# Performance work log

Hardware: AMD Instinct MI355X
Metric: run time of the kernel (lower is better)

The kernel has to match this reference:

```python
import jax, jax.numpy as jnp
import numpy as np

N_BITS = 8
LEVELS = 2 ** N_BITS - 1  # 255 quantization levels (asymmetric uniform)
EPS = 1e-8


def _round_ste(x):
    # straight-through round (forward: round, backward: identity)
    return x + jax.lax.stop_gradient(jnp.round(x) - x)


def _fake_quant_uniform(x):
    # dynamic per-tensor asymmetric uniform quantization (UniformQuantizer)
    xmin = jnp.min(x)
    xmax = jnp.max(x)
    scale = jnp.maximum((xmax - xmin) / LEVELS, EPS)
    zero_point = jnp.round(-xmin / scale)
    x_int = jnp.clip(_round_ste(x / scale) + zero_point, 0, LEVELS)
    return (x_int - zero_point) * scale


def setup_inputs() -> dict:
    key = jax.random.key(0)
    kA, kB = jax.random.split(key)
    A = jax.random.normal(kA, (4, 4096, 4096), dtype=jnp.float32)  # [batch, M, K]
    B = jax.random.normal(kB, (4096, 4096), dtype=jnp.float32)     # [K, N]
    return {"A": A, "B": B}


def reference(A, B):
    # QuantMatMul.forward with use_input_quant=True, use_weight_quant=True
    Aq = _fake_quant_uniform(A)
    Bq = _fake_quant_uniform(B)
    return Aq @ Bq  # [batch, M, N]
```

## Files before the change

kernel.cpp:

```cpp
#include <hip/hip_runtime.h>


#define K_DIM 4096
#define N_COLS 4096
#define M_ROWS 16384

typedef __attribute__((ext_vector_type(4))) int int4v;

struct QParams { float sa, zpa, sb, zpb, sab; int za, zb; };

static const size_t OFF_AQ = 0;
static const size_t OFF_BT = (size_t)64 << 20;
static const size_t OFF_RS = OFF_BT + ((size_t)16 << 20);
static const size_t OFF_CS = OFF_RS + (size_t)M_ROWS * 4;
static const size_t OFF_MM = OFF_CS + (size_t)N_COLS * 4;
static const size_t OFF_PR = OFF_MM + 64;

__device__ __forceinline__ unsigned enc_f(float f) {
  unsigned u = __float_as_uint(f);
  return (u & 0x80000000u) ? ~u : (u | 0x80000000u);
}
__device__ __forceinline__ float dec_f(unsigned e) {
  unsigned u = (e & 0x80000000u) ? (e & 0x7fffffffu) : ~e;
  return __uint_as_float(u);
}

__device__ __forceinline__ int quantize1(float x, float s, float zp) {
  return (int)(fminf(fmaxf(rintf(x / s) + zp, 0.0f), 255.0f)) - 128;
}

__device__ __forceinline__ void gload16(const void* g, void* l) {
  __builtin_amdgcn_global_load_lds(
      (const __attribute__((address_space(1))) unsigned int*)g,
      (__attribute__((address_space(3))) unsigned int*)l, 16, 0, 0);
}

__global__ void init_mm_k(unsigned* mm) {
  if (threadIdx.x == 0) {
    mm[0] = 0xFFFFFFFFu; mm[1] = 0u;
    mm[2] = 0xFFFFFFFFu; mm[3] = 0u;
  }
}

__global__ __launch_bounds__(256) void minmax_k(const float4* __restrict__ x, long n4,
                                                unsigned* __restrict__ mm) {
  float lo = 3.402823466e38f, hi = -3.402823466e38f;
  long i = (long)blockIdx.x * blockDim.x + threadIdx.x;
  const long stride = (long)gridDim.x * blockDim.x;
  for (; i < n4; i += stride) {
    float4 v = x[i];
    lo = fminf(lo, fminf(fminf(v.x, v.y), fminf(v.z, v.w)));
    hi = fmaxf(hi, fmaxf(fmaxf(v.x, v.y), fmaxf(v.z, v.w)));
  }
  for (int off = 32; off; off >>= 1) {
    lo = fminf(lo, __shfl_down(lo, off));
    hi = fmaxf(hi, __shfl_down(hi, off));
  }
  __shared__ float slo[4], shi[4];
  const int t = threadIdx.x;
  if ((t & 63) == 0) { slo[t >> 6] = lo; shi[t >> 6] = hi; }
  __syncthreads();
  if (t == 0) {
    for (int w = 1; w < 4; w++) { lo = fminf(lo, slo[w]); hi = fmaxf(hi, shi[w]); }
    atomicMin(&mm[0], enc_f(lo));
    atomicMax(&mm[1], enc_f(hi));
  }
}

__global__ void params_k(const unsigned* __restrict__ mm, QParams* __restrict__ p) {
  if (threadIdx.x != 0) return;
  const float amin = dec_f(mm[0]), amax = dec_f(mm[1]);
  const float bmin = dec_f(mm[2]), bmax = dec_f(mm[3]);
  const float sa = fmaxf((amax - amin) / 255.0f, 1e-8f);
  const float sb = fmaxf((bmax - bmin) / 255.0f, 1e-8f);
  const float zpa = rintf(-amin / sa);
  const float zpb = rintf(-bmin / sb);
  p->sa = sa; p->zpa = zpa; p->sb = sb; p->zpb = zpb;
  p->sab = sa * sb;
  p->za = (int)zpa - 128;
  p->zb = (int)zpb - 128;
}

__global__ __launch_bounds__(256) void quantA_k(const float* __restrict__ A,
                                                signed char* __restrict__ Aq,
                                                int* __restrict__ rowsum,
                                                const QParams* __restrict__ p) {
  const float sa = p->sa, zpa = p->zpa;
  const int row = blockIdx.x, t = threadIdx.x;
  const float4* src = (const float4*)(A + (size_t)row * K_DIM);
  unsigned* dst = (unsigned*)(Aq + (size_t)row * K_DIM);
  int sum = 0;
#pragma unroll
  for (int j = 0; j < 4; j++) {
    float4 v = src[j * 256 + t];
    int q0 = quantize1(v.x, sa, zpa);
    int q1 = quantize1(v.y, sa, zpa);
    int q2 = quantize1(v.z, sa, zpa);
    int q3 = quantize1(v.w, sa, zpa);
    sum += q0 + q1 + q2 + q3;
    dst[j * 256 + t] = ((unsigned)q0 & 255u) | (((unsigned)q1 & 255u) << 8) |
                       (((unsigned)q2 & 255u) << 16) | (((unsigned)q3 & 255u) << 24);
  }
  for (int off = 32; off; off >>= 1) sum += __shfl_down(sum, off);
  __shared__ int sw[4];
  if ((t & 63) == 0) sw[t >> 6] = sum;
  __syncthreads();
  if (t == 0) rowsum[row] = sw[0] + sw[1] + sw[2] + sw[3];
}

__global__ __launch_bounds__(256) void quantB_k(const float* __restrict__ B,
                                                signed char* __restrict__ Bt,
                                                const QParams* __restrict__ p) {
  const float sb = p->sb, zpb = p->zpb;
  __shared__ unsigned char s[64][72];
  const int n0 = blockIdx.x * 64, k0 = blockIdx.y * 64;
  const int t = threadIdx.x;
  const int kr = t >> 2, tl = t & 3;
  const float* rowp = B + (size_t)(k0 + kr) * N_COLS + n0;
#pragma unroll
  for (int j = 0; j < 4; j++) {
    const int fi = tl + j * 4;
    float4 v = *(const float4*)(rowp + fi * 4);
    int q0 = quantize1(v.x, sb, zpb);
    int q1 = quantize1(v.y, sb, zpb);
    int q2 = quantize1(v.z, sb, zpb);
    int q3 = quantize1(v.w, sb, zpb);
    *(unsigned*)&s[kr][fi * 4] = ((unsigned)q0 & 255u) | (((unsigned)q1 & 255u) << 8) |
                                 (((unsigned)q2 & 255u) << 16) | (((unsigned)q3 & 255u) << 24);
  }
  __syncthreads();
  const int nr = t >> 2, kb = tl * 16;
  unsigned w[4];
#pragma unroll
  for (int jj = 0; jj < 4; jj++) {
    unsigned b0 = s[kb + jj * 4 + 0][nr];
    unsigned b1 = s[kb + jj * 4 + 1][nr];
    unsigned b2 = s[kb + jj * 4 + 2][nr];
    unsigned b3 = s[kb + jj * 4 + 3][nr];
    w[jj] = b0 | (b1 << 8) | (b2 << 16) | (b3 << 24);
  }
  int4v o = {(int)w[0], (int)w[1], (int)w[2], (int)w[3]};
  *(int4v*)(Bt + (size_t)(n0 + nr) * K_DIM + k0 + kb) = o;
}

__global__ __launch_bounds__(256) void colsum_k(const signed char* __restrict__ Bt,
                                                int* __restrict__ colsum) {
  const int n = blockIdx.x, t = threadIdx.x;
  const int4v v = ((const int4v*)(Bt + (size_t)n * K_DIM))[t];
  int sum = 0;
#pragma unroll
  for (int c = 0; c < 4; c++) {
    unsigned w = (unsigned)v[c];
    sum += (int)(signed char)(w & 255u) + (int)(signed char)((w >> 8) & 255u) +
           (int)(signed char)((w >> 16) & 255u) + (int)(signed char)((w >> 24) & 255u);
  }
  for (int off = 32; off; off >>= 1) sum += __shfl_down(sum, off);
  __shared__ int sw[4];
  if ((t & 63) == 0) sw[t >> 6] = sum;
  __syncthreads();
  if (t == 0) colsum[n] = sw[0] + sw[1] + sw[2] + sw[3];
}

__global__ __launch_bounds__(256) void gemm_k(const signed char* __restrict__ Aq,
                                              const signed char* __restrict__ Bt,
                                              float* __restrict__ C,
                                              const int* __restrict__ rowsum,
                                              const int* __restrict__ colsum,
                                              const QParams* __restrict__ p) {
  __shared__ signed char As[128 * 64];
  __shared__ signed char Bs[128 * 64];
  const int t = threadIdx.x;
  const int m0 = blockIdx.y * 128, n0 = blockIdx.x * 128;
  const int w = t >> 6, l = t & 63;
  const int wm = (w & 1) * 64, wn = (w >> 1) * 64;
  const int ml = l & 15, q = l >> 4;

  int4v acc[4][4] = {};

  const int off0 = t * 16;
  const int srow = off0 >> 6, scol = off0 & 63;
  const signed char* gA = Aq + (size_t)(m0 + srow) * K_DIM + scol;
  const signed char* gB = Bt + (size_t)(n0 + srow) * K_DIM + scol;
  signed char* lA = As + off0;
  signed char* lB = Bs + off0;

  const signed char* pa = As + (wm + ml) * 64 + q * 16;
  const signed char* pb = Bs + (wn + ml) * 64 + q * 16;

  for (int kt = 0; kt < 64; kt++) {
    const size_t kof = (size_t)kt * 64;
    gload16(gA + kof, lA);
    gload16(gA + (size_t)64 * K_DIM + kof, lA + 4096);
    gload16(gB + kof, lB);
    gload16(gB + (size_t)64 * K_DIM + kof, lB + 4096);
    __syncthreads();

    int4v a[4], b[4];
#pragma unroll
    for (int i = 0; i < 4; i++) a[i] = *(const int4v*)(pa + i * 1024);
#pragma unroll
    for (int j = 0; j < 4; j++) b[j] = *(const int4v*)(pb + j * 1024);
#pragma unroll
    for (int i = 0; i < 4; i++)
#pragma unroll
      for (int j = 0; j < 4; j++)
        acc[i][j] = __builtin_amdgcn_mfma_i32_16x16x64_i8(a[i], b[j], acc[i][j], 0, 0, 0);
    __syncthreads();
  }

  const float sab = p->sab;
  const int za = p->za, zb = p->zb;
  const int kzz = K_DIM * za * zb;
  const int gm0 = m0 + wm + q * 4;
  const int gnb = n0 + wn + ml;
  int cs[4];
#pragma unroll
  for (int j = 0; j < 4; j++) cs[j] = za * colsum[gnb + j * 16];
#pragma unroll
  for (int i = 0; i < 4; i++) {
    int rs[4];
#pragma unroll
    for (int r = 0; r < 4; r++) rs[r] = zb * rowsum[gm0 + i * 16 + r];
#pragma unroll
    for (int j = 0; j < 4; j++) {
#pragma unroll
      for (int r = 0; r < 4; r++) {
        const int v = acc[i][j][r] - rs[r] - cs[j] + kzz;
        C[(size_t)(gm0 + i * 16 + r) * N_COLS + (gnb + j * 16)] = sab * (float)v;
      }
    }
  }
}

extern "C" void kernel_launch(void* const* d_in, const int* in_sizes, int n_in,
                              void* d_out, int out_size, void* d_ws, size_t ws_size,
                              hipStream_t stream) {
  const float* A = (const float*)d_in[0];
  const float* B = (const float*)d_in[1];
  float* C = (float*)d_out;
  char* ws = (char*)d_ws;
  signed char* Aq = (signed char*)(ws + OFF_AQ);
  signed char* Bt = (signed char*)(ws + OFF_BT);
  int* rowsum = (int*)(ws + OFF_RS);
  int* colsum = (int*)(ws + OFF_CS);
  unsigned* mm = (unsigned*)(ws + OFF_MM);
  QParams* prm = (QParams*)(ws + OFF_PR);

  init_mm_k<<<1, 64, 0, stream>>>(mm);
  minmax_k<<<4096, 256, 0, stream>>>((const float4*)A, (long)M_ROWS * K_DIM / 4, mm + 0);
  minmax_k<<<2048, 256, 0, stream>>>((const float4*)B, (long)K_DIM * N_COLS / 4, mm + 2);
  params_k<<<1, 64, 0, stream>>>(mm, prm);
  quantA_k<<<M_ROWS, 256, 0, stream>>>(A, Aq, rowsum, prm);
  quantB_k<<<dim3(64, 64), 256, 0, stream>>>(B, Bt, prm);
  colsum_k<<<N_COLS, 256, 0, stream>>>(Bt, colsum);
  gemm_k<<<dim3(32, 128), 256, 0, stream>>>(Aq, Bt, C, rowsum, colsum, prm);
}
```

Measured before the change: 956.7 us.

## Switch GEMM to 32x32x32 int8 MFMA with K=128 tiles and swizzled layout

The GEMM now uses 32x32x32 int8 MFMA instructions with a 128-wide K tile, which halves the number of K iterations and barriers. The quantize kernels write A and B with an XOR swizzle over 16-byte chunks so the LDS reads avoid bank conflicts. The two minmax launches are merged into one grid, and the quantizers multiply by a precomputed reciprocal instead of dividing. Multiplying by the reciprocal can round differently from true division for a few values, and colsum still sums the swizzled rows, which is fine because the sum is order-independent.

```diff
diff --git a/kernel.cpp b/kernel.cpp
--- a/kernel.cpp
+++ b/kernel.cpp
@@ -6,8 +6,9 @@
 #define M_ROWS 16384
 
 typedef __attribute__((ext_vector_type(4))) int int4v;
-
-struct QParams { float sa, zpa, sb, zpb, sab; int za, zb; };
+typedef __attribute__((ext_vector_type(16))) int int16v;
+
+struct QParams { float sa, zpa, sb, zpb, sab, ra, rb; int za, zb; };
 
 static const size_t OFF_AQ = 0;
 static const size_t OFF_BT = (size_t)64 << 20;
@@ -25,8 +26,8 @@
   return __uint_as_float(u);
 }
 
-__device__ __forceinline__ int quantize1(float x, float s, float zp) {
-  return (int)(fminf(fmaxf(rintf(x / s) + zp, 0.0f), 255.0f)) - 128;
+__device__ __forceinline__ int quantize1(float x, float r, float zp) {
+  return (int)(fminf(fmaxf(rintf(x * r) + zp, 0.0f), 255.0f)) - 128;
 }
 
 __device__ __forceinline__ void gload16(const void* g, void* l) {
@@ -42,11 +43,19 @@
   }
 }
 
-__global__ __launch_bounds__(256) void minmax_k(const float4* __restrict__ x, long n4,
+__global__ __launch_bounds__(256) void minmax_k(const float4* __restrict__ A,
+                                                const float4* __restrict__ B,
                                                 unsigned* __restrict__ mm) {
+  const bool isB = blockIdx.x >= 4096;
+  const float4* __restrict__ x = isB ? B : A;
+  const long n4 = isB ? (long)K_DIM * N_COLS / 4 : (long)M_ROWS * K_DIM / 4;
+  const int nblk = isB ? 1024 : 4096;
+  const int bid = isB ? (int)blockIdx.x - 4096 : (int)blockIdx.x;
+  unsigned* m = mm + (isB ? 2 : 0);
+
   float lo = 3.402823466e38f, hi = -3.402823466e38f;
-  long i = (long)blockIdx.x * blockDim.x + threadIdx.x;
-  const long stride = (long)gridDim.x * blockDim.x;
+  long i = (long)bid * blockDim.x + threadIdx.x;
+  const long stride = (long)nblk * blockDim.x;
   for (; i < n4; i += stride) {
     float4 v = x[i];
     lo = fminf(lo, fminf(fminf(v.x, v.y), fminf(v.z, v.w)));
@@ -62,8 +71,8 @@
   __syncthreads();
   if (t == 0) {
     for (int w = 1; w < 4; w++) { lo = fminf(lo, slo[w]); hi = fmaxf(hi, shi[w]); }
-    atomicMin(&mm[0], enc_f(lo));
-    atomicMax(&mm[1], enc_f(hi));
+    atomicMin(&m[0], enc_f(lo));
+    atomicMax(&m[1], enc_f(hi));
   }
 }
 
@@ -77,6 +86,8 @@
   const float zpb = rintf(-bmin / sb);
   p->sa = sa; p->zpa = zpa; p->sb = sb; p->zpb = zpb;
   p->sab = sa * sb;
+  p->ra = 1.0f / sa;
+  p->rb = 1.0f / sb;
   p->za = (int)zpa - 128;
   p->zb = (int)zpb - 128;
 }
@@ -85,21 +96,23 @@
                                                 signed char* __restrict__ Aq,
                                                 int* __restrict__ rowsum,
                                                 const QParams* __restrict__ p) {
-  const float sa = p->sa, zpa = p->zpa;
+  const float ra = p->ra, zpa = p->zpa;
   const int row = blockIdx.x, t = threadIdx.x;
   const float4* src = (const float4*)(A + (size_t)row * K_DIM);
   unsigned* dst = (unsigned*)(Aq + (size_t)row * K_DIM);
   int sum = 0;
 #pragma unroll
   for (int j = 0; j < 4; j++) {
-    float4 v = src[j * 256 + t];
-    int q0 = quantize1(v.x, sa, zpa);
-    int q1 = quantize1(v.y, sa, zpa);
-    int q2 = quantize1(v.z, sa, zpa);
-    int q3 = quantize1(v.w, sa, zpa);
+    const int d = j * 256 + t;
+    float4 v = src[d];
+    int q0 = quantize1(v.x, ra, zpa);
+    int q1 = quantize1(v.y, ra, zpa);
+    int q2 = quantize1(v.z, ra, zpa);
+    int q3 = quantize1(v.w, ra, zpa);
     sum += q0 + q1 + q2 + q3;
-    dst[j * 256 + t] = ((unsigned)q0 & 255u) | (((unsigned)q1 & 255u) << 8) |
-                       (((unsigned)q2 & 255u) << 16) | (((unsigned)q3 & 255u) << 24);
+    const int dsw = (d & ~0x1C) | ((((d >> 2) ^ row) & 7) << 2);
+    dst[dsw] = ((unsigned)q0 & 255u) | (((unsigned)q1 & 255u) << 8) |
+               (((unsigned)q2 & 255u) << 16) | (((unsigned)q3 & 255u) << 24);
   }
   for (int off = 32; off; off >>= 1) sum += __shfl_down(sum, off);
   __shared__ int sw[4];
@@ -111,7 +124,7 @@
 __global__ __launch_bounds__(256) void quantB_k(const float* __restrict__ B,
                                                 signed char* __restrict__ Bt,
                                                 const QParams* __restrict__ p) {
-  const float sb = p->sb, zpb = p->zpb;
+  const float rb = p->rb, zpb = p->zpb;
   __shared__ unsigned char s[64][72];
   const int n0 = blockIdx.x * 64, k0 = blockIdx.y * 64;
   const int t = threadIdx.x;
@@ -121,15 +134,16 @@
   for (int j = 0; j < 4; j++) {
     const int fi = tl + j * 4;
     float4 v = *(const float4*)(rowp + fi * 4);
-    int q0 = quantize1(v.x, sb, zpb);
-    int q1 = quantize1(v.y, sb, zpb);
-    int q2 = quantize1(v.z, sb, zpb);
-    int q3 = quantize1(v.w, sb, zpb);
+    int q0 = quantize1(v.x, rb, zpb);
+    int q1 = quantize1(v.y, rb, zpb);
+    int q2 = quantize1(v.z, rb, zpb);
+    int q3 = quantize1(v.w, rb, zpb);
     *(unsigned*)&s[kr][fi * 4] = ((unsigned)q0 & 255u) | (((unsigned)q1 & 255u) << 8) |
                                  (((unsigned)q2 & 255u) << 16) | (((unsigned)q3 & 255u) << 24);
   }
   __syncthreads();
-  const int nr = t >> 2, kb = tl * 16;
+  const int nr = t >> 2;
+  const int kb = tl * 16;
   unsigned w[4];
 #pragma unroll
   for (int jj = 0; jj < 4; jj++) {
@@ -140,7 +154,9 @@
     w[jj] = b0 | (b1 << 8) | (b2 << 16) | (b3 << 24);
   }
   int4v o = {(int)w[0], (int)w[1], (int)w[2], (int)w[3]};
-  *(int4v*)(Bt + (size_t)(n0 + nr) * K_DIM + k0 + kb) = o;
+  const int bo = k0 + kb;
+  const int bsw = (bo & ~0x70) | ((((bo >> 4) ^ nr) & 7) << 4);
+  *(int4v*)(Bt + (size_t)(n0 + nr) * K_DIM + bsw) = o;
 }
 
 __global__ __launch_bounds__(256) void colsum_k(const signed char* __restrict__ Bt,
@@ -161,72 +177,67 @@
   if (t == 0) colsum[n] = sw[0] + sw[1] + sw[2] + sw[3];
 }
 
-__global__ __launch_bounds__(256) void gemm_k(const signed char* __restrict__ Aq,
-                                              const signed char* __restrict__ Bt,
-                                              float* __restrict__ C,
-                                              const int* __restrict__ rowsum,
-                                              const int* __restrict__ colsum,
-                                              const QParams* __restrict__ p) {
-  __shared__ signed char As[128 * 64];
-  __shared__ signed char Bs[128 * 64];
+__global__ __launch_bounds__(256, 4) void gemm_k(const signed char* __restrict__ Aq,
+                                                 const signed char* __restrict__ Bt,
+                                                 float* __restrict__ C,
+                                                 const int* __restrict__ rowsum,
+                                                 const int* __restrict__ colsum,
+                                                 const QParams* __restrict__ p) {
+  __shared__ signed char As[128 * 128];
+  __shared__ signed char Bs[128 * 128];
   const int t = threadIdx.x;
   const int m0 = blockIdx.y * 128, n0 = blockIdx.x * 128;
   const int w = t >> 6, l = t & 63;
   const int wm = (w & 1) * 64, wn = (w >> 1) * 64;
-  const int ml = l & 15, q = l >> 4;
-
-  int4v acc[4][4] = {};
-
-  const int off0 = t * 16;
-  const int srow = off0 >> 6, scol = off0 & 63;
+  const int r32 = l & 31, h = l >> 5;
+
+  int16v acc[2][2] = {};
+
+  const int off = t * 16;
+  const int srow = off >> 7, scol = off & 127;
   const signed char* gA = Aq + (size_t)(m0 + srow) * K_DIM + scol;
   const signed char* gB = Bt + (size_t)(n0 + srow) * K_DIM + scol;
-  signed char* lA = As + off0;
-  signed char* lB = Bs + off0;
-
-  const signed char* pa = As + (wm + ml) * 64 + q * 16;
-  const signed char* pb = Bs + (wn + ml) * 64 + q * 16;
-
-  for (int kt = 0; kt < 64; kt++) {
-    const size_t kof = (size_t)kt * 64;
-    gload16(gA + kof, lA);
-    gload16(gA + (size_t)64 * K_DIM + kof, lA + 4096);
-    gload16(gB + kof, lB);
-    gload16(gB + (size_t)64 * K_DIM + kof, lB + 4096);
+
+  const int swz = (r32 & 7);
+
+  for (int kt = 0; kt < 32; kt++) {
+    const size_t kof = (size_t)kt * 128;
+#pragma unroll
+    for (int r = 0; r < 4; r++) {
+      gload16(gA + (size_t)(32 * r) * K_DIM + kof, As + off + r * 4096);
+      gload16(gB + (size_t)(32 * r) * K_DIM + kof, Bs + off + r * 4096);
+    }
     __syncthreads();
-
-    int4v a[4], b[4];
-#pragma unroll
-    for (int i = 0; i < 4; i++) a[i] = *(const int4v*)(pa + i * 1024);
-#pragma unroll
-    for (int j = 0; j < 4; j++) b[j] = *(const int4v*)(pb + j * 1024);
-#pragma unroll
-    for (int i = 0; i < 4; i++)
-#pragma unroll
-      for (int j = 0; j < 4; j++)
-        acc[i][j] = __builtin_amdgcn_mfma_i32_16x16x64_i8(a[i], b[j], acc[i][j], 0, 0, 0);
+#pragma unroll
+    for (int s = 0; s < 4; s++) {
+      const int ca = ((2 * s + h) ^ swz) << 4;
+      int4v a0 = *(const int4v*)(As + (wm + r32) * 128 + ca);
+      int4v a1 = *(const int4v*)(As + (wm + 32 + r32) * 128 + ca);
+      int4v b0 = *(const int4v*)(Bs + (wn + r32) * 128 + ca);
+      int4v b1 = *(const int4v*)(Bs + (wn + 32 + r32) * 128 + ca);
+      acc[0][0] = __builtin_amdgcn_mfma_i32_32x32x32_i8(a0, b0, acc[0][0], 0, 0, 0);
+      acc[0][1] = __builtin_amdgcn_mfma_i32_32x32x32_i8(a0, b1, acc[0][1], 0, 0, 0);
+      acc[1][0] = __builtin_amdgcn_mfma_i32_32x32x32_i8(a1, b0, acc[1][0], 0, 0, 0);
+      acc[1][1] = __builtin_amdgcn_mfma_i32_32x32x32_i8(a1, b1, acc[1][1], 0, 0, 0);
+    }
     __syncthreads();
   }
 
   const float sab = p->sab;
   const int za = p->za, zb = p->zb;
   const int kzz = K_DIM * za * zb;
-  const int gm0 = m0 + wm + q * 4;
-  const int gnb = n0 + wn + ml;
-  int cs[4];
-#pragma unroll
-  for (int j = 0; j < 4; j++) cs[j] = za * colsum[gnb + j * 16];
-#pragma unroll
-  for (int i = 0; i < 4; i++) {
-    int rs[4];
-#pragma unroll
-    for (int r = 0; r < 4; r++) rs[r] = zb * rowsum[gm0 + i * 16 + r];
-#pragma unroll
-    for (int j = 0; j < 4; j++) {
-#pragma unroll
-      for (int r = 0; r < 4; r++) {
-        const int v = acc[i][j][r] - rs[r] - cs[j] + kzz;
-        C[(size_t)(gm0 + i * 16 + r) * N_COLS + (gnb + j * 16)] = sab * (float)v;
+#pragma unroll
+  for (int j = 0; j < 2; j++) {
+    const int col = n0 + wn + j * 32 + r32;
+    const int cs = za * colsum[col];
+#pragma unroll
+    for (int i = 0; i < 2; i++) {
+      const int rbase = m0 + wm + i * 32 + 4 * h;
+#pragma unroll
+      for (int r = 0; r < 16; r++) {
+        const int row = rbase + (r & 3) + 8 * (r >> 2);
+        const int v = acc[i][j][r] - zb * rowsum[row] - cs + kzz;
+        C[(size_t)row * N_COLS + col] = sab * (float)v;
       }
     }
   }
@@ -247,8 +258,7 @@
   QParams* prm = (QParams*)(ws + OFF_PR);
 
   init_mm_k<<<1, 64, 0, stream>>>(mm);
-  minmax_k<<<4096, 256, 0, stream>>>((const float4*)A, (long)M_ROWS * K_DIM / 4, mm + 0);
-  minmax_k<<<2048, 256, 0, stream>>>((const float4*)B, (long)K_DIM * N_COLS / 4, mm + 2);
+  minmax_k<<<5120, 256, 0, stream>>>((const float4*)A, (const float4*)B, mm);
   params_k<<<1, 64, 0, stream>>>(mm, prm);
   quantA_k<<<M_ROWS, 256, 0, stream>>>(A, Aq, rowsum, prm);
   quantB_k<<<dim3(64, 64), 256, 0, stream>>>(B, Bt, prm);
```

New measurement: 869.2 us. 9.1% less time.
